# Kernel tuning notes

Measured on AMD Instinct MI355X. Metric: run time of the kernel, lower is better.

Reference implementation:

```python
import jax, jax.numpy as jnp
import numpy as np

B, T, D_IN, D_OUT, H = 4, 2048, 768, 768, 12
HD = D_OUT // H  # 64


def setup_inputs() -> dict:
    key = jax.random.key(0)
    ks = jax.random.split(key, 6)
    s_in = 1.0 / np.sqrt(D_IN)
    s_out = 1.0 / np.sqrt(D_OUT)
    return {
        "x": jax.random.normal(ks[0], (B, T, D_IN), dtype=jnp.float32),
        "Wq": jax.random.uniform(ks[1], (D_IN, D_OUT), jnp.float32, -s_in, s_in),
        "Wk": jax.random.uniform(ks[2], (D_IN, D_OUT), jnp.float32, -s_in, s_in),
        "Wv": jax.random.uniform(ks[3], (D_IN, D_OUT), jnp.float32, -s_in, s_in),
        "Wo": jax.random.uniform(ks[4], (D_OUT, D_OUT), jnp.float32, -s_out, s_out),
        "bo": jax.random.uniform(ks[5], (D_OUT,), jnp.float32, -s_out, s_out),
    }


def reference(x, Wq, Wk, Wv, Wo, bo):
    b, t, _ = x.shape
    # QKV projections (no bias, per qkv_bias=False), split into heads: [b,h,t,hd]
    q = (x @ Wq).reshape(b, t, H, HD).transpose(0, 2, 1, 3)
    k = (x @ Wk).reshape(b, t, H, HD).transpose(0, 2, 1, 3)
    v = (x @ Wv).reshape(b, t, H, HD).transpose(0, 2, 1, 3)
    # NOTE: original calls masked_fill (non-in-place) and discards the result,
    # so NO causal mask is actually applied. Faithfully reproduce that.
    scores = jnp.einsum("bhqd,bhkd->bhqk", q, k)  # [b,h,t,t]
    attn = jax.nn.softmax(scores / jnp.sqrt(jnp.float32(HD)), axis=-1)
    # dropout p=0.0 (eval) -> identity
    ctx = jnp.einsum("bhqk,bhkd->bhqd", attn, v)  # [b,h,t,hd]
    ctx = ctx.transpose(0, 2, 1, 3).reshape(b, t, D_OUT)
    return ctx @ Wo + bo
```

## Files before the change

### kernel.cpp

```cpp
#include <hip/hip_runtime.h>
#include <hip/hip_bf16.h>
#include <stdint.h>


#define HH   12
#define TT   2048
#define DIN  768
#define DOUT 768
#define HD   64
#define BB   4
#define MTOT (BB*TT)
#define NQKV (3*DOUT)
#define QSCALE 0.1803368801111832f

typedef float  float4v  __attribute__((ext_vector_type(4)));
typedef float  float16v __attribute__((ext_vector_type(16)));
typedef __bf16 bf16x8   __attribute__((ext_vector_type(8)));
typedef short  short8v  __attribute__((ext_vector_type(8)));

#define AS1 __attribute__((address_space(1)))
#define AS3 __attribute__((address_space(3)))

static __device__ __forceinline__ void gload_lds16(const void* g, void* l) {
    __builtin_amdgcn_global_load_lds((AS1 void*)g, (AS3 void*)l, 16, 0, 0);
}

static __device__ __forceinline__ short f2bf(float f) {
    __bf16 h = (__bf16)f;
    return __builtin_bit_cast(short, h);
}

__global__ __launch_bounds__(256) void cast_x_kernel(const float* __restrict__ x,
                                                     short* __restrict__ xb, int n4) {
    int i = blockIdx.x * 256 + threadIdx.x;
    if (i >= n4) return;
    float4 v = ((const float4*)x)[i];
    short4 o;
    o.x = f2bf(v.x); o.y = f2bf(v.y); o.z = f2bf(v.z); o.w = f2bf(v.w);
    ((short4*)xb)[i] = o;
}

__global__ __launch_bounds__(256) void prep_w_kernel(const float* __restrict__ Wq,
                                                     const float* __restrict__ Wk,
                                                     const float* __restrict__ Wv,
                                                     const float* __restrict__ Wo,
                                                     short* __restrict__ Wqkvt,
                                                     short* __restrict__ Wot) {
    __shared__ short tile[32 * 33];
    const int bx = blockIdx.x, by = blockIdx.y, bz = blockIdx.z;
    const float* W = (bz == 0) ? Wq : (bz == 1) ? Wk : (bz == 2) ? Wv : Wo;
    const int tx = threadIdx.x & 31, ty = threadIdx.x >> 5;
    for (int i = 0; i < 4; i++) {
        int k = by * 32 + ty + i * 8;
        tile[(ty + i * 8) * 33 + tx] = f2bf(W[(size_t)k * DOUT + bx * 32 + tx]);
    }
    __syncthreads();
    for (int i = 0; i < 4; i++) {
        int n = bx * 32 + ty + i * 8;
        int k = by * 32 + tx;
        short v = tile[tx * 33 + ty + i * 8];
        if (bz < 3) Wqkvt[(size_t)(bz * DOUT + n) * DIN + k] = v;
        else        Wot[(size_t)n * DOUT + k] = v;
    }
}

__global__ __launch_bounds__(256) void qkv_gemm_kernel(const short* __restrict__ Xb,
                                                       const short* __restrict__ Wt,
                                                       short* __restrict__ Qb,
                                                       short* __restrict__ Kb,
                                                       short* __restrict__ Vt) {
    __shared__ __align__(16) short lds[16384];
    short* ldsA = lds;
    short* ldsB = lds + 4096;
    const int t = threadIdx.x;
    const int w = t >> 6, lane = t & 63;
    const int quad = lane >> 4, l15 = lane & 15;
    const int m0 = blockIdx.x * 128, n0 = blockIdx.y * 128;
    const int wm = (w >> 1) * 64, wn = (w & 1) * 64;

    float4v acc[4][4];
    for (int i = 0; i < 4; i++)
        for (int j = 0; j < 4; j++)
            acc[i][j] = (float4v)0.0f;

    const int rA = t >> 2;
    const int cSw = ((t & 3) ^ ((t >> 3) & 3)) * 8;
    const short* gA0 = Xb + (size_t)(m0 + rA) * DIN + cSw;
    const short* gB0 = Wt + (size_t)(n0 + rA) * DIN + cSw;
    const int pos = (quad ^ ((l15 >> 1) & 3)) * 8;

    for (int k0 = 0; k0 < DIN; k0 += 32) {
        gload_lds16(gA0 + k0,            &ldsA[t * 8]);
        gload_lds16(gA0 + 64 * DIN + k0, &ldsA[(t + 256) * 8]);
        gload_lds16(gB0 + k0,            &ldsB[t * 8]);
        gload_lds16(gB0 + 64 * DIN + k0, &ldsB[(t + 256) * 8]);
        __syncthreads();
        bf16x8 af[4], bfr[4];
        for (int i = 0; i < 4; i++) af[i]  = *(const bf16x8*)&ldsA[(wm + i * 16 + l15) * 32 + pos];
        for (int j = 0; j < 4; j++) bfr[j] = *(const bf16x8*)&ldsB[(wn + j * 16 + l15) * 32 + pos];
        for (int i = 0; i < 4; i++)
            for (int j = 0; j < 4; j++)
                acc[i][j] = __builtin_amdgcn_mfma_f32_16x16x32_bf16(af[i], bfr[j], acc[i][j], 0, 0, 0);
        __syncthreads();
    }

    const int which = n0 / DOUT;
    if (which < 2) {
        short* ldsT = lds;
        const float sc = (which == 0) ? QSCALE : 1.0f;
        short* dst = (which == 0) ? Qb : Kb;
        const int n0sec = n0 - which * DOUT;
        for (int i = 0; i < 4; i++)
            for (int j = 0; j < 4; j++) {
                int col = wn + j * 16 + l15;
                int cx = col >> 3, co = col & 7;
                for (int r = 0; r < 4; r++) {
                    int row = wm + i * 16 + quad * 4 + r;
                    ldsT[row * 128 + ((cx ^ (row & 7)) * 8 + co)] = f2bf(acc[i][j][r] * sc);
                }
            }
        __syncthreads();
        for (int p = 0; p < 8; p++) {
            int row = p * 16 + (t >> 4);
            int cL = t & 15;
            short8v v = *(const short8v*)&ldsT[row * 128 + ((cL ^ (row & 7)) * 8)];
            int mg = m0 + row;
            int b2 = mg >> 11, tq = mg & 2047;
            int colg = n0sec + cL * 8;
            int hh = colg >> 6, d = colg & 63;
            *(short8v*)&dst[((size_t)((b2 * HH + hh) * TT + tq) << 6) + d] = v;
        }
    } else {
        short* ldsT = lds;
        const int n0r = n0 - 2 * DOUT;
        const int b = m0 >> 11, tq0 = m0 & 2047;
        for (int i = 0; i < 4; i++)
            for (int j = 0; j < 4; j++)
                for (int r = 0; r < 4; r++) {
                    int nl = wn + j * 16 + l15;
                    int ml = wm + i * 16 + quad * 4 + r;
                    int c = ml >> 3, o = ml & 7;
                    ldsT[nl * 128 + ((c ^ (nl & 7)) * 8 + o)] = f2bf(acc[i][j][r]);
                }
        __syncthreads();
        for (int p = 0; p < 8; p++) {
            int nrow = p * 16 + (t >> 4);
            int cc = t & 15;
            short8v v = *(const short8v*)&ldsT[nrow * 128 + ((cc ^ (nrow & 7)) * 8)];
            int colg = n0r + nrow;
            int hh = colg >> 6, d = colg & 63;
            *(short8v*)&Vt[(size_t)((b * HH + hh) * HD + d) * TT + tq0 + cc * 8] = v;
        }
    }
}

__global__ __launch_bounds__(256, 3) void attn_kernel(const short* __restrict__ Qb,
                                                      const short* __restrict__ Kb,
                                                      const short* __restrict__ Vt,
                                                      short* __restrict__ Ctx) {
    __shared__ __align__(16) short ldsK[2][64 * 64];
    __shared__ __align__(16) short ldsV[2][64 * 64];
    const int t = threadIdx.x;
    const int w = t >> 6, lane = t & 63;
    const int half = lane >> 5, m = lane & 31;
    const int bh = blockIdx.x;
    const int b = bh / HH, h = bh - b * HH;
    const int q0 = blockIdx.y * 128 + w * 32;

    const short* Qbase = Qb + (size_t)bh * TT * HD;
    const short* Kbase = Kb + (size_t)bh * TT * HD;
    const short* Vbase = Vt + (size_t)bh * HD * TT;

    bf16x8 qf[4];
#pragma unroll
    for (int s = 0; s < 4; s++)
        qf[s] = *(const bf16x8*)&Qbase[(q0 + m) * HD + s * 16 + half * 8];

    int kOff[2], vOff[2];
    {
        int r5 = t >> 3;
        int pi = ((r5 >> 3) & 1) * 16 + ((r5 >> 2) & 1) * 8 + ((r5 >> 4) & 1) * 4 + (r5 & 3);
#pragma unroll
        for (int g = 0; g < 2; g++) {
            kOff[g] = (g * 32 + pi) * 64 + (((t & 7) ^ (r5 & 7)) * 8);
            int vrow = g * 32 + r5;
            vOff[g] = vrow * TT + (((t & 7) ^ (vrow & 7)) * 8);
        }
    }

    auto stage = [&](int buf, int u0) {
#pragma unroll
        for (int g = 0; g < 2; g++)
            gload_lds16(Kbase + (size_t)u0 * 64 + kOff[g], &ldsK[buf][(g * 256 + t) * 8]);
#pragma unroll
        for (int g = 0; g < 2; g++)
            gload_lds16(Vbase + (size_t)u0 + vOff[g], &ldsV[buf][(g * 256 + t) * 8]);
    };

    float16v accO[2];
    accO[0] = (float16v)0.0f;
    accO[1] = (float16v)0.0f;
    float lsum = 0.0f;

    stage(0, 0);

    for (int it = 0; it < TT / 64; ++it) {
        __syncthreads();
        const int buf = it & 1;
        if (it + 1 < TT / 64) stage(buf ^ 1, (it + 1) * 64);
        const short* K_ = &ldsK[buf][0];
        const short* V_ = &ldsV[buf][0];

#pragma unroll
        for (int kt = 0; kt < 2; kt++) {
            float16v st = (float16v)0.0f;
#pragma unroll
            for (int s = 0; s < 4; s++) {
                bf16x8 ka = *(const bf16x8*)&K_[(kt * 32 + m) * 64 + (((s * 2 + half) ^ (m & 7)) * 8)];
                st = __builtin_amdgcn_mfma_f32_32x32x16_bf16(ka, qf[s], st, 0, 0, 0);
            }
            float pe[16];
#pragma unroll
            for (int i = 0; i < 16; i++) pe[i] = __builtin_amdgcn_exp2f(st[i]);
            float s01 = 0.0f;
#pragma unroll
            for (int i = 0; i < 16; i++) s01 += pe[i];
            lsum += s01;
            bf16x8 ap[2];
#pragma unroll
            for (int i = 0; i < 4; i++) {
                ap[0][i]     = (__bf16)pe[i];
                ap[0][4 + i] = (__bf16)pe[8 + i];
                ap[1][i]     = (__bf16)pe[4 + i];
                ap[1][4 + i] = (__bf16)pe[12 + i];
            }
#pragma unroll
            for (int ks = 0; ks < 2; ks++)
#pragma unroll
                for (int dt = 0; dt < 2; dt++) {
                    int row = dt * 32 + m;
                    bf16x8 bv = *(const bf16x8*)&V_[row * 64 + (((kt * 4 + ks * 2 + half) ^ (row & 7)) * 8)];
                    accO[dt] = __builtin_amdgcn_mfma_f32_32x32x16_bf16(ap[ks], bv, accO[dt], 0, 0, 0);
                }
        }
    }

    {
        float v = lsum + __shfl_xor(lsum, 32);
        float linv = 1.0f / v;
#pragma unroll
        for (int s = 0; s < 4; s++)
#pragma unroll
            for (int i = 0; i < 4; i++) {
                int reg = s * 4 + i;
                int qrow = i + s * 8 + half * 4;
                float ln = __shfl(linv, qrow);
                int qg = q0 + qrow;
                size_t base = (size_t)(b * TT + qg) * DOUT + h * HD + m;
                Ctx[base]      = f2bf(accO[0][reg] * ln);
                Ctx[base + 32] = f2bf(accO[1][reg] * ln);
            }
    }
}

__global__ __launch_bounds__(256) void out_gemm_kernel(const short* __restrict__ Cb,
                                                       const short* __restrict__ Wot,
                                                       const float* __restrict__ bo,
                                                       float* __restrict__ out) {
    __shared__ __align__(16) short ldsA[64 * 32];
    __shared__ __align__(16) short ldsB[128 * 32];
    const int t = threadIdx.x;
    const int w = t >> 6, lane = t & 63;
    const int quad = lane >> 4, l15 = lane & 15;
    const int m0 = blockIdx.x * 64, n0 = blockIdx.y * 128;
    const int wn = w * 32;

    float4v acc[4][2];
    for (int i = 0; i < 4; i++)
        for (int j = 0; j < 2; j++)
            acc[i][j] = (float4v)0.0f;

    const int rA = t >> 2;
    const int cSw = ((t & 3) ^ ((t >> 3) & 3)) * 8;
    const short* gA0 = Cb + (size_t)(m0 + rA) * DOUT + cSw;
    const short* gB0 = Wot + (size_t)(n0 + rA) * DOUT + cSw;
    const int pos = (quad ^ ((l15 >> 1) & 3)) * 8;

    for (int k0 = 0; k0 < DOUT; k0 += 32) {
        gload_lds16(gA0 + k0,             &ldsA[t * 8]);
        gload_lds16(gB0 + k0,             &ldsB[t * 8]);
        gload_lds16(gB0 + 64 * DOUT + k0, &ldsB[(t + 256) * 8]);
        __syncthreads();
        bf16x8 af[4], bfr[2];
        for (int i = 0; i < 4; i++) af[i]  = *(const bf16x8*)&ldsA[(i * 16 + l15) * 32 + pos];
        for (int j = 0; j < 2; j++) bfr[j] = *(const bf16x8*)&ldsB[(wn + j * 16 + l15) * 32 + pos];
        for (int i = 0; i < 4; i++)
            for (int j = 0; j < 2; j++)
                acc[i][j] = __builtin_amdgcn_mfma_f32_16x16x32_bf16(af[i], bfr[j], acc[i][j], 0, 0, 0);
        __syncthreads();
    }

    for (int i = 0; i < 4; i++) {
        int m = m0 + i * 16 + quad * 4;
        for (int j = 0; j < 2; j++) {
            int n = n0 + wn + j * 16 + l15;
            float bias = bo[n];
            for (int r = 0; r < 4; r++)
                out[(size_t)(m + r) * DOUT + n] = acc[i][j][r] + bias;
        }
    }
}

extern "C" void kernel_launch(void* const* d_in, const int* in_sizes, int n_in,
                              void* d_out, int out_size, void* d_ws, size_t ws_size,
                              hipStream_t stream) {
    const float* x  = (const float*)d_in[0];
    const float* Wq = (const float*)d_in[1];
    const float* Wk = (const float*)d_in[2];
    const float* Wv = (const float*)d_in[3];
    const float* Wo = (const float*)d_in[4];
    const float* bo = (const float*)d_in[5];
    float* out = (float*)d_out;

    char* ws = (char*)d_ws;
    short* Xb    = (short*)(ws + 0);
    short* Wqkvt = (short*)(ws + 12582912);
    short* Wot   = (short*)(ws + 16121856);
    short* Qb    = (short*)(ws + 17301504);
    short* Kb    = (short*)(ws + 29884416);
    short* Vt    = (short*)(ws + 42467328);
    short* Cb    = (short*)(ws + 55050240);

    cast_x_kernel<<<(MTOT * DIN / 4 + 255) / 256, 256, 0, stream>>>(x, Xb, MTOT * DIN / 4);
    prep_w_kernel<<<dim3(24, 24, 4), 256, 0, stream>>>(Wq, Wk, Wv, Wo, Wqkvt, Wot);
    qkv_gemm_kernel<<<dim3(MTOT / 128, NQKV / 128), 256, 0, stream>>>(Xb, Wqkvt, Qb, Kb, Vt);
    attn_kernel<<<dim3(BB * HH, TT / 128), 256, 0, stream>>>(Qb, Kb, Vt, Cb);
    out_gemm_kernel<<<dim3(MTOT / 64, DOUT / 128), 256, 0, stream>>>(Cb, Wot, bo, out);
}
```

Baseline: 212.6 us.

## Process 64 query rows per wave in attention, halving block size to 128 threads

Each attention wave now handles two 32-row query tiles, so every K and V fragment read from LDS feeds two MFMAs instead of one. Blocks shrink to two waves (128 threads) that still cover 128 queries, and each thread issues twice as many async global-to-LDS loads per stage. s_setprio is raised around the MFMA sections to favour matrix issue over the exp/convert work. This doubles accumulator and Q-fragment registers per wave and lowers the waves per block, which can reduce latency hiding and occupancy.

```diff
diff --git a/kernel.cpp b/kernel.cpp
--- a/kernel.cpp
+++ b/kernel.cpp
@@ -154,7 +154,7 @@
     }
 }
 
-__global__ __launch_bounds__(256, 3) void attn_kernel(const short* __restrict__ Qb,
+__global__ __launch_bounds__(128, 2) void attn_kernel(const short* __restrict__ Qb,
                                                       const short* __restrict__ Kb,
                                                       const short* __restrict__ Vt,
                                                       short* __restrict__ Ctx) {
@@ -165,42 +165,51 @@
     const int half = lane >> 5, m = lane & 31;
     const int bh = blockIdx.x;
     const int b = bh / HH, h = bh - b * HH;
-    const int q0 = blockIdx.y * 128 + w * 32;
+    const int q0 = blockIdx.y * 128 + w * 64;
 
     const short* Qbase = Qb + (size_t)bh * TT * HD;
     const short* Kbase = Kb + (size_t)bh * TT * HD;
     const short* Vbase = Vt + (size_t)bh * HD * TT;
 
-    bf16x8 qf[4];
-#pragma unroll
-    for (int s = 0; s < 4; s++)
-        qf[s] = *(const bf16x8*)&Qbase[(q0 + m) * HD + s * 16 + half * 8];
-
-    int kOff[2], vOff[2];
+    bf16x8 qf[2][4];
+#pragma unroll
+    for (int qh = 0; qh < 2; qh++)
+#pragma unroll
+        for (int s = 0; s < 4; s++)
+            qf[qh][s] = *(const bf16x8*)&Qbase[(q0 + qh * 32 + m) * HD + s * 16 + half * 8];
+
+    int kOff[4], vOff[4], uD[4];
     {
-        int r5 = t >> 3;
-        int pi = ((r5 >> 3) & 1) * 16 + ((r5 >> 2) & 1) * 8 + ((r5 >> 4) & 1) * 4 + (r5 & 3);
-#pragma unroll
-        for (int g = 0; g < 2; g++) {
-            kOff[g] = (g * 32 + pi) * 64 + (((t & 7) ^ (r5 & 7)) * 8);
-            int vrow = g * 32 + r5;
-            vOff[g] = vrow * TT + (((t & 7) ^ (vrow & 7)) * 8);
+#pragma unroll
+        for (int g = 0; g < 4; g++) {
+            int u = g * 128 + t;
+            int gg = u >> 8;
+            int r5 = (u >> 3) & 31;
+            int c = u & 7;
+            int pi = ((r5 >> 3) & 1) * 16 + ((r5 >> 2) & 1) * 8 + ((r5 >> 4) & 1) * 4 + (r5 & 3);
+            kOff[g] = (gg * 32 + pi) * 64 + ((c ^ (r5 & 7)) * 8);
+            int vrow = gg * 32 + r5;
+            vOff[g] = vrow * TT + ((c ^ (vrow & 7)) * 8);
+            uD[g] = u * 8;
         }
     }
 
     auto stage = [&](int buf, int u0) {
 #pragma unroll
-        for (int g = 0; g < 2; g++)
-            gload_lds16(Kbase + (size_t)u0 * 64 + kOff[g], &ldsK[buf][(g * 256 + t) * 8]);
-#pragma unroll
-        for (int g = 0; g < 2; g++)
-            gload_lds16(Vbase + (size_t)u0 + vOff[g], &ldsV[buf][(g * 256 + t) * 8]);
+        for (int g = 0; g < 4; g++)
+            gload_lds16(Kbase + (size_t)u0 * 64 + kOff[g], &ldsK[buf][uD[g]]);
+#pragma unroll
+        for (int g = 0; g < 4; g++)
+            gload_lds16(Vbase + (size_t)u0 + vOff[g], &ldsV[buf][uD[g]]);
     };
 
-    float16v accO[2];
-    accO[0] = (float16v)0.0f;
-    accO[1] = (float16v)0.0f;
-    float lsum = 0.0f;
+    float16v accO[2][2];
+#pragma unroll
+    for (int qh = 0; qh < 2; qh++)
+#pragma unroll
+        for (int dt = 0; dt < 2; dt++)
+            accO[qh][dt] = (float16v)0.0f;
+    float lsum[2] = {0.0f, 0.0f};
 
     stage(0, 0);
 
@@ -213,40 +222,54 @@
 
 #pragma unroll
         for (int kt = 0; kt < 2; kt++) {
-            float16v st = (float16v)0.0f;
+            float16v st0 = (float16v)0.0f;
+            float16v st1 = (float16v)0.0f;
+            __builtin_amdgcn_s_setprio(1);
 #pragma unroll
             for (int s = 0; s < 4; s++) {
                 bf16x8 ka = *(const bf16x8*)&K_[(kt * 32 + m) * 64 + (((s * 2 + half) ^ (m & 7)) * 8)];
-                st = __builtin_amdgcn_mfma_f32_32x32x16_bf16(ka, qf[s], st, 0, 0, 0);
+                st0 = __builtin_amdgcn_mfma_f32_32x32x16_bf16(ka, qf[0][s], st0, 0, 0, 0);
+                st1 = __builtin_amdgcn_mfma_f32_32x32x16_bf16(ka, qf[1][s], st1, 0, 0, 0);
             }
-            float pe[16];
-#pragma unroll
-            for (int i = 0; i < 16; i++) pe[i] = __builtin_amdgcn_exp2f(st[i]);
-            float s01 = 0.0f;
-#pragma unroll
-            for (int i = 0; i < 16; i++) s01 += pe[i];
-            lsum += s01;
-            bf16x8 ap[2];
-#pragma unroll
-            for (int i = 0; i < 4; i++) {
-                ap[0][i]     = (__bf16)pe[i];
-                ap[0][4 + i] = (__bf16)pe[8 + i];
-                ap[1][i]     = (__bf16)pe[4 + i];
-                ap[1][4 + i] = (__bf16)pe[12 + i];
+            __builtin_amdgcn_s_setprio(0);
+
+            bf16x8 ap[2][2];
+#pragma unroll
+            for (int qh = 0; qh < 2; qh++) {
+                float pe[16];
+#pragma unroll
+                for (int i = 0; i < 16; i++)
+                    pe[i] = __builtin_amdgcn_exp2f(qh ? st1[i] : st0[i]);
+                float s01 = 0.0f;
+#pragma unroll
+                for (int i = 0; i < 16; i++) s01 += pe[i];
+                lsum[qh] += s01;
+#pragma unroll
+                for (int i = 0; i < 4; i++) {
+                    ap[qh][0][i]     = (__bf16)pe[i];
+                    ap[qh][0][4 + i] = (__bf16)pe[8 + i];
+                    ap[qh][1][i]     = (__bf16)pe[4 + i];
+                    ap[qh][1][4 + i] = (__bf16)pe[12 + i];
+                }
             }
+
+            __builtin_amdgcn_s_setprio(1);
 #pragma unroll
             for (int ks = 0; ks < 2; ks++)
 #pragma unroll
                 for (int dt = 0; dt < 2; dt++) {
                     int row = dt * 32 + m;
                     bf16x8 bv = *(const bf16x8*)&V_[row * 64 + (((kt * 4 + ks * 2 + half) ^ (row & 7)) * 8)];
-                    accO[dt] = __builtin_amdgcn_mfma_f32_32x32x16_bf16(ap[ks], bv, accO[dt], 0, 0, 0);
+                    accO[0][dt] = __builtin_amdgcn_mfma_f32_32x32x16_bf16(ap[0][ks], bv, accO[0][dt], 0, 0, 0);
+                    accO[1][dt] = __builtin_amdgcn_mfma_f32_32x32x16_bf16(ap[1][ks], bv, accO[1][dt], 0, 0, 0);
                 }
-        }
-    }
-
-    {
-        float v = lsum + __shfl_xor(lsum, 32);
+            __builtin_amdgcn_s_setprio(0);
+        }
+    }
+
+#pragma unroll
+    for (int qh = 0; qh < 2; qh++) {
+        float v = lsum[qh] + __shfl_xor(lsum[qh], 32);
         float linv = 1.0f / v;
 #pragma unroll
         for (int s = 0; s < 4; s++)
@@ -255,10 +278,10 @@
                 int reg = s * 4 + i;
                 int qrow = i + s * 8 + half * 4;
                 float ln = __shfl(linv, qrow);
-                int qg = q0 + qrow;
+                int qg = q0 + qh * 32 + qrow;
                 size_t base = (size_t)(b * TT + qg) * DOUT + h * HD + m;
-                Ctx[base]      = f2bf(accO[0][reg] * ln);
-                Ctx[base + 32] = f2bf(accO[1][reg] * ln);
+                Ctx[base]      = f2bf(accO[qh][0][reg] * ln);
+                Ctx[base + 32] = f2bf(accO[qh][1][reg] * ln);
             }
     }
 }
@@ -334,6 +357,6 @@
     cast_x_kernel<<<(MTOT * DIN / 4 + 255) / 256, 256, 0, stream>>>(x, Xb, MTOT * DIN / 4);
     prep_w_kernel<<<dim3(24, 24, 4), 256, 0, stream>>>(Wq, Wk, Wv, Wo, Wqkvt, Wot);
     qkv_gemm_kernel<<<dim3(MTOT / 128, NQKV / 128), 256, 0, stream>>>(Xb, Wqkvt, Qb, Kb, Vt);
-    attn_kernel<<<dim3(BB * HH, TT / 128), 256, 0, stream>>>(Qb, Kb, Vt, Cb);
+    attn_kernel<<<dim3(BB * HH, TT / 128), 128, 0, stream>>>(Qb, Kb, Vt, Cb);
     out_gemm_kernel<<<dim3(MTOT / 64, DOUT / 128), 256, 0, stream>>>(Cb, Wot, bo, out);
 }
```

Result: no change. 213.5 us (+0.4%).
